# Kernel optimization log

Hardware: AMD Instinct MI355X
Metric: run time of the kernel (lower is better)

## Reference

```python
import jax, jax.numpy as jnp
import numpy as np
from jax import lax

B, T, IN, H, NC = 512, 512, 128, 256, 10
GRID_SIZE, SPLINE_ORDER = 5, 3


def _grid(in_f):
    h = 2.0 / GRID_SIZE
    pts = jnp.arange(-SPLINE_ORDER, GRID_SIZE + SPLINE_ORDER + 1, dtype=jnp.float32) * h - 1.0
    return jnp.broadcast_to(pts, (in_f, pts.shape[0]))


def _b_splines(x, grid):
    # x: (B, in); grid: (in, GRID_SIZE + 2*SPLINE_ORDER + 1)
    xg = x[..., None]
    b = ((xg >= grid[:, :-1]) & (xg < grid[:, 1:])).astype(x.dtype)
    for k in range(1, SPLINE_ORDER + 1):
        b = ((xg - grid[:, :-(k + 1)]) / (grid[:, k:-1] - grid[:, :-(k + 1)]) * b[..., :-1]
             + (grid[:, k + 1:] - xg) / (grid[:, k + 1:] - grid[:, 1:-k]) * b[..., 1:])
    return b  # (B, in, GRID_SIZE + SPLINE_ORDER)


def _kan_linear(x, base_w, spline_w, scaler):
    g = _grid(x.shape[-1])
    base = jax.nn.silu(x) @ base_w.T
    spline = jnp.einsum('bik,oik->bo', _b_splines(x, g), spline_w * scaler[..., None])
    return base + spline


def _gru_cell(x, h, wih, whh, bih, bhh):
    gi = x @ wih.T + bih
    gh = h @ whh.T + bhh
    ir, iz, inn = jnp.split(gi, 3, axis=-1)
    hr, hz, hn = jnp.split(gh, 3, axis=-1)
    r = jax.nn.sigmoid(ir + hr)
    z = jax.nn.sigmoid(iz + hz)
    n = jnp.tanh(inn + r * hn)
    return (1.0 - z) * n + z * h


def _lstm_single(x, wih, whh, bih, bhh):
    # single-timestep LSTM with zero initial (h, c); gate order i,f,g,o
    h0 = jnp.zeros((x.shape[0], whh.shape[1]), x.dtype)
    g = x @ wih.T + h0 @ whh.T + bih + bhh
    i, f, gg, o = jnp.split(g, 4, axis=-1)
    c = jax.nn.sigmoid(i) * jnp.tanh(gg)
    return jax.nn.sigmoid(o) * jnp.tanh(c)


def setup_inputs() -> dict:
    keys = iter(jax.random.split(jax.random.key(0), 64))
    def w(*shape):
        return jax.random.normal(next(keys), shape, jnp.float32) * 0.1
    d = {}
    d['x'] = jax.random.normal(next(keys), (B, T, IN), jnp.float32)
    d['gru0_wih'] = w(3 * H, IN); d['gru0_whh'] = w(3 * H, H)
    d['gru0_bih'] = w(3 * H); d['gru0_bhh'] = w(3 * H)
    d['gru1_wih'] = w(3 * H, H); d['gru1_whh'] = w(3 * H, H)
    d['gru1_bih'] = w(3 * H); d['gru1_bhh'] = w(3 * H)
    for suf in ['0', '0r', '1', '1r']:
        d['lw_ih' + suf] = w(512, 256); d['lw_hh' + suf] = w(512, 128)
        d['lb_ih' + suf] = w(512); d['lb_hh' + suf] = w(512)
    d['kan1_base'] = w(64, 256); d['kan1_spline'] = w(64, 256, GRID_SIZE + SPLINE_ORDER); d['kan1_scaler'] = w(64, 256)
    d['kan2_base'] = w(NC, 64); d['kan2_spline'] = w(NC, 64, GRID_SIZE + SPLINE_ORDER); d['kan2_scaler'] = w(NC, 64)
    return d


def reference(x, gru0_wih, gru0_whh, gru0_bih, gru0_bhh, gru1_wih, gru1_whh, gru1_bih, gru1_bhh,
              lw_ih0, lw_hh0, lb_ih0, lb_hh0, lw_ih0r, lw_hh0r, lb_ih0r, lb_hh0r,
              lw_ih1, lw_hh1, lb_ih1, lb_hh1, lw_ih1r, lw_hh1r, lb_ih1r, lb_hh1r,
              kan1_base, kan1_spline, kan1_scaler, kan2_base, kan2_spline, kan2_scaler):
    bsz = x.shape[0]
    h_init = (jnp.zeros((bsz, H), x.dtype), jnp.zeros((bsz, H), x.dtype))

    def step(carry, xt):
        h0, h1 = carry
        h0 = _gru_cell(xt, h0, gru0_wih, gru0_whh, gru0_bih, gru0_bhh)
        h1 = _gru_cell(h0, h1, gru1_wih, gru1_whh, gru1_bih, gru1_bhh)
        return (h0, h1), None

    (h0, h1), _ = lax.scan(step, h_init, jnp.swapaxes(x, 0, 1))  # time-major scan
    s = h1  # last layer final hidden, seq_len-1 single step for LSTM
    o0 = jnp.concatenate([_lstm_single(s, lw_ih0, lw_hh0, lb_ih0, lb_hh0),
                          _lstm_single(s, lw_ih0r, lw_hh0r, lb_ih0r, lb_hh0r)], axis=-1)
    o1 = jnp.concatenate([_lstm_single(o0, lw_ih1, lw_hh1, lb_ih1, lb_hh1),
                          _lstm_single(o0, lw_ih1r, lw_hh1r, lb_ih1r, lb_hh1r)], axis=-1)
    z = _kan_linear(o1, kan1_base, kan1_spline, kan1_scaler)
    return _kan_linear(z, kan2_base, kan2_spline, kan2_scaler)
```

## Files before the change

kernel.cpp:

```cpp
#include <hip/hip_runtime.h>
#include <stdint.h>


constexpr int B_  = 512;
constexpr int T_  = 512;
constexpr int IN_ = 128;
constexpr int H_  = 256;
constexpr int GR_ = 32;
constexpr int PL_ = GR_ * 2 * 4096;
constexpr int TCp = 64;
constexpr int NCp = 8;

typedef __attribute__((ext_vector_type(8))) short bf16x8;
typedef __attribute__((ext_vector_type(4))) float f32x4;

#define MFMA16(a, b, c) __builtin_amdgcn_mfma_f32_16x16x32_bf16((a), (b), (c), 0, 0, 0)

__device__ __forceinline__ float bf2f(unsigned short u){
    union { unsigned int i; float f; } v; v.i = ((unsigned int)u) << 16; return v.f;
}
__device__ __forceinline__ unsigned short f2bf(float f){
    union { float f; unsigned int i; } v; v.f = f;
    return (unsigned short)((v.i + 0x7FFFu + ((v.i >> 16) & 1u)) >> 16);
}
__device__ __forceinline__ unsigned int cvtpk(float a, float b){
    unsigned int r;
    asm("v_cvt_pk_bf16_f32 %0, %1, %2" : "=v"(r) : "v"(a), "v"(b));
    return r;
}
__device__ __forceinline__ unsigned long long pk4(float a, float b, float c, float d){
    const unsigned int lo = cvtpk(a, b), hi = cvtpk(c, d);
    return (unsigned long long)lo | ((unsigned long long)hi << 32);
}
__device__ __forceinline__ float sig_(float x){
    return __builtin_amdgcn_rcpf(1.0f + __expf(-x));
}
__device__ __forceinline__ float tanh_(float x){
    return 1.0f - 2.0f * __builtin_amdgcn_rcpf(1.0f + __expf(2.0f * x));
}
__device__ __forceinline__ bf16x8 ldb8g(const unsigned short* p){ return *(const bf16x8*)p; }

union U64x2 { unsigned long long q[2]; bf16x8 v; };

__device__ __forceinline__ void gl2lds16(const void* g, void* l){
    __builtin_amdgcn_global_load_lds(
        (const __attribute__((address_space(1))) unsigned int*)g,
        (__attribute__((address_space(3))) unsigned int*)l, 16, 0, 0);
}

__global__ void srt_detect(const unsigned int* __restrict__ xw, unsigned int* __restrict__ flag){
    int cnt = 0;
    for (int i = threadIdx.x; i < 1024; i += 64){
        const unsigned int lo = xw[i] & 0xFFFFu;
        const int e = (int)((lo >> 7) & 0xFFu);
        if (e >= 100 && e <= 140) cnt++;
    }
    #pragma unroll
    for (int o = 32; o > 0; o >>= 1) cnt += __shfl_down(cnt, o);
    if (threadIdx.x == 0) *flag = (cnt > 614) ? 1u : 0u;
}

struct ConvTab { const void* src[26]; int n[26]; int off[26]; };

__global__ __launch_bounds__(256) void srt_conv(ConvTab ct, unsigned short* __restrict__ wb,
                                                const unsigned int* __restrict__ flag){
    const bool isb = (*flag != 0);
    const int gsz = gridDim.x * blockDim.x;
    const int gid = blockIdx.x * blockDim.x + threadIdx.x;
    for (int j = 0; j < 26; ++j){
        const int n = ct.n[j];
        unsigned short* o = wb + ct.off[j];
        if (isb){
            const unsigned short* s = (const unsigned short*)ct.src[j];
            for (int i = gid; i < n; i += gsz) o[i] = s[i];
        } else {
            const float* s = (const float*)ct.src[j];
            for (int i = gid; i < n; i += gsz) o[i] = f2bf(s[i]);
        }
    }
}

__global__ __launch_bounds__(256) void srt_prep(
    float* __restrict__ h0s, float* __restrict__ h1s,
    float* __restrict__ bias0, float* __restrict__ bias1,
    const unsigned short* __restrict__ b0ih, const unsigned short* __restrict__ b0hh,
    const unsigned short* __restrict__ b1ih, const unsigned short* __restrict__ b1hh,
    unsigned int* __restrict__ seq)
{
    const int gid = blockIdx.x * blockDim.x + threadIdx.x;
    h0s[gid] = 0.f;
    h1s[gid] = 0.f;
    if (gid < 768){
        bias0[gid] = bf2f(b0ih[gid]) + (gid < 512 ? bf2f(b0hh[gid]) : 0.f);
        bias1[gid] = bf2f(b1ih[gid]) + (gid < 512 ? bf2f(b1hh[gid]) : 0.f);
    }
    if (gid < 1024) seq[gid] = 0u;
}

__device__ void seq_dev(unsigned short* shm,
    const unsigned short* __restrict__ gi,
    const unsigned short* __restrict__ whh,
    const unsigned short* __restrict__ bhh,
    float* __restrict__ hstate,
    unsigned short* __restrict__ h_all,
    const int TC, const int bg)
{
    unsigned short* wnL   = shm;
    unsigned short* hbufB = shm + 32768;
    unsigned short* gibB  = shm + 32768 + 8192;

    const int tid  = threadIdx.x;
    const int lane = tid & 63;
    const int wv   = tid >> 6;
    const int l15  = lane & 15;
    const int quad = lane >> 4;
    const int m0   = bg * 16;
    const int swz  = (l15 & 7) << 4;

    bf16x8 wr[5][8];
    #pragma unroll
    for (int fi = 0; fi < 6; ++fi){
        const int u = fi >> 1, ii = fi & 1;
        const unsigned short* wp =
            whh + (size_t)(u * 256 + wv * 32 + ii * 16 + l15) * 256 + quad * 8;
        if (fi < 5){
            #pragma unroll
            for (int kc = 0; kc < 8; ++kc) wr[fi][kc] = ldb8g(wp + kc * 32);
        } else {
            #pragma unroll
            for (int kc = 0; kc < 8; ++kc)
                *(bf16x8*)&wnL[((wv * 8 + kc) << 9) + lane * 8] = ldb8g(wp + kc * 32);
        }
    }

    f32x4 bn0[2];
    #pragma unroll
    for (int ii = 0; ii < 2; ++ii)
        #pragma unroll
        for (int j = 0; j < 4; ++j)
            bn0[ii][j] = bf2f(bhh[512 + wv * 32 + ii * 16 + quad * 4 + j]);

    f32x4 hr[2];
    #pragma unroll
    for (int ii = 0; ii < 2; ++ii)
        hr[ii] = *(const f32x4*)&hstate[(size_t)(m0 + l15) * 256 + wv * 32 + ii * 16 + quad * 4];

    const unsigned short* gpp[3]; int gdl[3];
    #pragma unroll
    for (int i = 0; i < 3; ++i){
        const int g_  = i * 512 + tid;
        const int row = g_ / 96;
        const int cg  = g_ - row * 96;
        gpp[i] = gi + ((size_t)m0 + row) * 768 + ((cg ^ (row & 7)) << 3);
        gdl[i] = g_ * 8;
    }

    #pragma unroll
    for (int ii = 0; ii < 2; ++ii){
        const unsigned long long pk = pk4(hr[ii][0], hr[ii][1], hr[ii][2], hr[ii][3]);
        *(unsigned long long*)((char*)hbufB + l15 * 512 +
            ((wv * 64 + ii * 32 + quad * 8) ^ swz)) = pk;
    }
    #pragma unroll
    for (int i = 0; i < 3; ++i) gl2lds16(gpp[i], &gibB[gdl[i]]);
    __syncthreads();

    #pragma unroll 1
    for (int t = 0; t < TC; ++t){
        const int par = t & 1;
        unsigned short* hb_cur = hbufB + par * 4096;
        unsigned short* hb_nxt = hbufB + (par ^ 1) * 4096;
        unsigned short* gb_cur = gibB + par * 12288;
        unsigned short* gb_nxt = gibB + (par ^ 1) * 12288;

        if (t + 1 < TC){
            const size_t toff = (size_t)(t + 1) * (512 * 768);
            #pragma unroll
            for (int i = 0; i < 3; ++i) gl2lds16(gpp[i] + toff, &gb_nxt[gdl[i]]);
        }

        f32x4 aR0 = {0,0,0,0}, aR1 = {0,0,0,0}, aZ0 = {0,0,0,0}, aZ1 = {0,0,0,0};
        f32x4 aN0 = bn0[0], aN1 = bn0[1];
        __builtin_amdgcn_s_setprio(1);
        #pragma unroll
        for (int kc = 0; kc < 8; ++kc){
            const bf16x8 hb = *(const bf16x8*)((const char*)hb_cur +
                l15 * 512 + ((kc * 64 + quad * 16) ^ swz));
            const bf16x8 w5 = *(const bf16x8*)&wnL[((wv * 8 + kc) << 9) + lane * 8];
            aR0 = MFMA16(wr[0][kc], hb, aR0);
            aR1 = MFMA16(wr[1][kc], hb, aR1);
            aZ0 = MFMA16(wr[2][kc], hb, aZ0);
            aZ1 = MFMA16(wr[3][kc], hb, aZ1);
            aN0 = MFMA16(wr[4][kc], hb, aN0);
            aN1 = MFMA16(w5,        hb, aN1);
        }
        __builtin_amdgcn_s_setprio(0);

        const char* gbase = (const char*)gb_cur + l15 * 1536;
        #pragma unroll
        for (int ii = 0; ii < 2; ++ii){
            const int cb = wv * 64 + ii * 32 + quad * 8;
            const unsigned long long qr = *(const unsigned long long*)(gbase + ((       cb) ^ swz));
            const unsigned long long qz = *(const unsigned long long*)(gbase + ((512  + cb) ^ swz));
            const unsigned long long qn = *(const unsigned long long*)(gbase + ((1024 + cb) ^ swz));
            const f32x4 aR = ii ? aR1 : aR0;
            const f32x4 aZ = ii ? aZ1 : aZ0;
            const f32x4 aN = ii ? aN1 : aN0;
            #pragma unroll
            for (int j = 0; j < 4; ++j){
                const float rr = sig_(aR[j] + bf2f((unsigned short)(qr >> (16 * j))));
                const float zz = sig_(aZ[j] + bf2f((unsigned short)(qz >> (16 * j))));
                const float nn = tanh_(bf2f((unsigned short)(qn >> (16 * j))) + rr * aN[j]);
                hr[ii][j] = (1.0f - zz) * nn + zz * hr[ii][j];
            }
        }

        #pragma unroll
        for (int ii = 0; ii < 2; ++ii){
            const unsigned long long pk = pk4(hr[ii][0], hr[ii][1], hr[ii][2], hr[ii][3]);
            *(unsigned long long*)((char*)hb_nxt + l15 * 512 +
                ((wv * 64 + ii * 32 + quad * 8) ^ swz)) = pk;
            if (h_all)
                *(unsigned long long*)(h_all + ((size_t)t * 512 + m0 + l15) * 256 +
                    wv * 32 + ii * 16 + quad * 4) = pk;
        }

        __syncthreads();
    }

    #pragma unroll
    for (int ii = 0; ii < 2; ++ii)
        *(f32x4*)&hstate[(size_t)(m0 + l15) * 256 + wv * 32 + ii * 16 + quad * 4] = hr[ii];
}

template<int K, bool XS>
__device__ void gemm_dev(unsigned short* shm, const void* Asrc, const bool isb,
                         const int t0, const unsigned short* __restrict__ W,
                         const float* __restrict__ bias,
                         unsigned short* __restrict__ C,
                         const int nb, const int mg)
{
    unsigned short* Wt = shm;
    unsigned short* Ab = shm + 64 * K;

    const int tid = threadIdx.x;
    const int lane = tid & 63, wv = tid >> 6;
    const int l15 = lane & 15, quad = lane >> 4;
    const int fh = wv & 1, mq = wv >> 1;
    constexpr int NK  = K / 64;
    constexpr int GW  = K / 8;
    constexpr int WG  = 64 * GW / 512;
    constexpr int NIT = 32 * NK;

    #pragma unroll
    for (int i = 0; i < WG; ++i){
        const int g_ = i * 512 + tid;
        const int row = g_ / GW, cg = g_ % GW;
        gl2lds16(W + (size_t)(nb * 64 + row) * K + ((cg ^ (row & 7)) << 3), &Wt[g_ * 8]);
    }

    float bs[2][4];
    #pragma unroll
    for (int ni = 0; ni < 2; ++ni)
        #pragma unroll
        for (int j = 0; j < 4; ++j)
            bs[ni][j] = bias[nb * 64 + fh * 32 + ni * 16 + quad * 4 + j];

    auto stageA = [&](int it){
        const int mt = it / NK, kk = it % NK;
        unsigned short* dst = Ab + (it & 1) * 8192;
        #pragma unroll
        for (int i = 0; i < 2; ++i){
            const int g_ = i * 512 + tid;
            const int row = g_ >> 3, cg = g_ & 7;
            const int r = mg * 4096 + mt * 128 + row;
            if (XS){
                const int b = r & 511, tt = r >> 9;
                const size_t s0 = ((size_t)b * 512 + (t0 + tt)) * 128 + kk * 64;
                if (isb){
                    gl2lds16((const unsigned short*)Asrc + s0 + ((cg ^ (row & 7)) << 3),
                             &dst[g_ * 8]);
                } else {
                    const float* p = (const float*)Asrc + s0 + cg * 8;
                    const float4 f0 = *(const float4*)p;
                    const float4 f1 = *(const float4*)(p + 4);
                    uint4 u;
                    u.x = cvtpk(f0.x, f0.y); u.y = cvtpk(f0.z, f0.w);
                    u.z = cvtpk(f1.x, f1.y); u.w = cvtpk(f1.z, f1.w);
                    *(uint4*)&dst[(row * 8 + (cg ^ (row & 7))) * 8] = u;
                }
            } else {
                gl2lds16((const unsigned short*)Asrc + (size_t)r * K + kk * 64 +
                         ((cg ^ (row & 7)) << 3), &dst[g_ * 8]);
            }
        }
    };

    stageA(0);
    __syncthreads();

    bf16x8 wf[2][2 * NK];
    #pragma unroll
    for (int ni = 0; ni < 2; ++ni)
        #pragma unroll
        for (int k2 = 0; k2 < 2 * NK; ++k2){
            const int rf = fh * 32 + ni * 16 + l15;
            wf[ni][k2] = *(const bf16x8*)((const char*)Wt +
                rf * (2 * K) + (((k2 * 4 + quad) ^ (rf & 7)) << 4));
        }

    #pragma unroll 1
    for (int mt = 0; mt < 32; ++mt){
        f32x4 acc[2][2];
        #pragma unroll
        for (int ni = 0; ni < 2; ++ni){
            acc[ni][0] = (f32x4){0,0,0,0};
            acc[ni][1] = (f32x4){0,0,0,0};
        }

        #pragma unroll
        for (int kk = 0; kk < NK; ++kk){
            const int it = mt * NK + kk;
            if (it) __syncthreads();
            if (it + 1 < NIT) stageA(it + 1);

            const char* ab = (const char*)(Ab + (it & 1) * 8192);
            #pragma unroll
            for (int kc = 0; kc < 2; ++kc){
                bf16x8 af[2];
                #pragma unroll
                for (int mi = 0; mi < 2; ++mi){
                    const int ra = mq * 32 + mi * 16 + l15;
                    af[mi] = *(const bf16x8*)(ab + ra * 128 +
                              (((kc * 4 + quad) ^ (ra & 7)) << 4));
                }
                #pragma unroll
                for (int ni = 0; ni < 2; ++ni)
                    #pragma unroll
                    for (int mi = 0; mi < 2; ++mi)
                        acc[ni][mi] = MFMA16(wf[ni][kk * 2 + kc], af[mi], acc[ni][mi]);
            }
        }

        #pragma unroll
        for (int ni = 0; ni < 2; ++ni)
            #pragma unroll
            for (int mi = 0; mi < 2; ++mi){
                const unsigned int lo = cvtpk(acc[ni][mi][0] + bs[ni][0],
                                              acc[ni][mi][1] + bs[ni][1]);
                const unsigned int hi = cvtpk(acc[ni][mi][2] + bs[ni][2],
                                              acc[ni][mi][3] + bs[ni][3]);
                const int row = mg * 4096 + mt * 128 + mq * 32 + mi * 16 + l15;
                const int col = nb * 64 + fh * 32 + ni * 16 + quad * 4;
                uint2 st; st.x = lo; st.y = hi;
                *(uint2*)(C + (size_t)row * 768 + col) = st;
            }
    }
}

struct PA {
    const void* xv;
    const unsigned int* flag;
    const unsigned short *w0ih, *w0hh, *b0hh, *w1ih, *w1hh, *b1hh;
    const float *bias0, *bias1;
    float *h0s, *h1s;
    unsigned short *gi0a, *gi0b, *haa, *hab, *gi1a, *gi1b;
    int p;
};

__global__ __launch_bounds__(512, 1) void srt_phase(PA a){
    __shared__ __align__(16) unsigned short shm[65536];
    const int bid = blockIdx.x;
    const int p = a.p;

    if (bid < 32){
        const int c = p - 1; if (c < 0 || c >= NCp) return;
        seq_dev(shm, (c & 1) ? a.gi0b : a.gi0a, a.w0hh, a.b0hh, a.h0s,
                (c & 1) ? a.hab : a.haa, TCp, bid);
    } else if (bid < 64){
        const int c = p - 3; if (c < 0 || c >= NCp) return;
        seq_dev(shm, (c & 1) ? a.gi1b : a.gi1a, a.w1hh, a.b1hh, a.h1s,
                nullptr, TCp, bid - 32);
    } else if (bid < 160){
        const int c = p; if (c >= NCp) return;
        const bool isb = (*a.flag != 0);
        const int idx = bid - 64;
        gemm_dev<128, true>(shm, a.xv, isb, c * TCp, a.w0ih, a.bias0,
                            (c & 1) ? a.gi0b : a.gi0a, idx % 12, idx / 12);
    } else {
        const int c = p - 2; if (c < 0 || c >= NCp) return;
        const int idx = bid - 160;
        gemm_dev<256, false>(shm, (c & 1) ? a.hab : a.haa, true, 0, a.w1ih, a.bias1,
                             (c & 1) ? a.gi1b : a.gi1a, idx % 12, idx / 12);
    }
}

__global__ __launch_bounds__(256, 1) void srt_gru(
    const void* __restrict__ xv,
    const unsigned short* __restrict__ w0ih,
    const unsigned short* __restrict__ w0hh,
    const unsigned short* __restrict__ b0ih,
    const unsigned short* __restrict__ b0hh,
    const unsigned short* __restrict__ w1ih,
    const unsigned short* __restrict__ w1hh,
    const unsigned short* __restrict__ b1ih,
    const unsigned short* __restrict__ b1hh,
    float* __restrict__ s_out,
    const unsigned int* __restrict__ flagp,
    unsigned int* __restrict__ seq,
    unsigned short* __restrict__ hb)
{
    __shared__ __align__(16) unsigned short w0hhL[4 * 24 * 512];

    const bool isb = (*flagp != 0);
    const int tid  = threadIdx.x;
    const int lane = tid & 63;
    const int wv   = tid >> 6;
    const int l15  = lane & 15;
    const int quad = lane >> 4;
    const int q    = blockIdx.x >> 5;
    const int g    = blockIdx.x & 31;
    const int m0   = g * 16;
    const int c    = q * 64 + wv * 16 + l15;

    bf16x8 w0ihr[3][4];
    #pragma unroll
    for (int u = 0; u < 3; ++u)
        #pragma unroll
        for (int kc = 0; kc < 4; ++kc)
            w0ihr[u][kc] = ldb8g(w0ih + (u * 256 + c) * IN_ + kc * 32 + quad * 8);

    bf16x8 w1ihr[3][8], w1hhr[3][8];
    #pragma unroll
    for (int u = 0; u < 3; ++u)
        #pragma unroll
        for (int kc = 0; kc < 8; ++kc){
            w1ihr[u][kc] = ldb8g(w1ih + (u * 256 + c) * H_ + kc * 32 + quad * 8);
            w1hhr[u][kc] = ldb8g(w1hh + (u * 256 + c) * H_ + kc * 32 + quad * 8);
        }

    const int wl = wv * 12288 + lane * 8;
    #pragma unroll
    for (int u = 0; u < 3; ++u)
        #pragma unroll
        for (int kc = 0; kc < 8; ++kc){
            const bf16x8 f = ldb8g(w0hh + (u * 256 + c) * H_ + kc * 32 + quad * 8);
            *(bf16x8*)&w0hhL[wl + (u * 8 + kc) * 512] = f;
        }

    const float brz0a = bf2f(b0ih[c])       + bf2f(b0hh[c]);
    const float brz0b = bf2f(b0ih[256 + c]) + bf2f(b0hh[256 + c]);
    const float bni0v = bf2f(b0ih[512 + c]);
    const float bnh0v = bf2f(b0hh[512 + c]);
    const float brz1a = bf2f(b1ih[c])       + bf2f(b1hh[c]);
    const float brz1b = bf2f(b1ih[256 + c]) + bf2f(b1hh[256 + c]);
    const float bni1v = bf2f(b1ih[512 + c]);
    const float bnh1v = bf2f(b1hh[512 + c]);
    __syncthreads();

    float h0r[4] = {0.f, 0.f, 0.f, 0.f};
    float h1r[4] = {0.f, 0.f, 0.f, 0.f};

    const size_t xrow = (size_t)(m0 + l15) * (T_ * IN_) + quad * 8;
    const unsigned short* pxb = (const unsigned short*)xv + xrow;
    const float*          pxf = (const float*)xv + xrow;

    unsigned int* sq = seq + g * 32;
    const int wr_row[4] = {(quad * 4 + 0) * 256 + c, (quad * 4 + 1) * 256 + c,
                           (quad * 4 + 2) * 256 + c, (quad * 4 + 3) * 256 + c};

    const f32x4 z4 = {0.f, 0.f, 0.f, 0.f};
    bf16x8 h0A[8], h1A[8];
    #pragma unroll
    for (int kc = 0; kc < 8; ++kc){
        h0A[kc] = (bf16x8)(short)0;
        h1A[kc] = (bf16x8)(short)0;
    }

    #pragma unroll 1
    for (int t = 0; t < T_; ++t){
        const int par = t & 1;
        const unsigned int tgt = 4u * (unsigned)(t + 1);
        unsigned short* plane = hb + par * PL_ + g * (2 * 4096);

        #pragma unroll
        for (int j = 0; j < 4; ++j)
            __hip_atomic_store(&plane[4096 + wr_row[j]], f2bf(h1r[j]),
                               __ATOMIC_RELAXED, __HIP_MEMORY_SCOPE_AGENT);

        bf16x8 ax[4];
        if (isb){
            #pragma unroll
            for (int kc = 0; kc < 4; ++kc) ax[kc] = ldb8g(pxb + t * IN_ + kc * 32);
        } else {
            #pragma unroll
            for (int kc = 0; kc < 4; ++kc){
                const float* p = pxf + t * IN_ + kc * 32;
                const float4 f0 = *(const float4*)p;
                const float4 f1 = *(const float4*)(p + 4);
                bf16x8 a;
                a[0] = (short)f2bf(f0.x); a[1] = (short)f2bf(f0.y);
                a[2] = (short)f2bf(f0.z); a[3] = (short)f2bf(f0.w);
                a[4] = (short)f2bf(f1.x); a[5] = (short)f2bf(f1.y);
                a[6] = (short)f2bf(f1.z); a[7] = (short)f2bf(f1.w);
                ax[kc] = a;
            }
        }

        f32x4 Tr = z4, Tz = z4, Tni = z4, Tnh = z4;
        #pragma unroll
        for (int kc = 0; kc < 4; ++kc){
            Tr  = MFMA16(ax[kc], w0ihr[0][kc], Tr);
            Tz  = MFMA16(ax[kc], w0ihr[1][kc], Tz);
            Tni = MFMA16(ax[kc], w0ihr[2][kc], Tni);
        }
        #pragma unroll
        for (int kc = 0; kc < 8; ++kc){
            const bf16x8 a = h0A[kc];
            Tr  = MFMA16(a, *(const bf16x8*)&w0hhL[wl + (0 * 8 + kc) * 512], Tr);
            Tz  = MFMA16(a, *(const bf16x8*)&w0hhL[wl + (1 * 8 + kc) * 512], Tz);
            Tnh = MFMA16(a, *(const bf16x8*)&w0hhL[wl + (2 * 8 + kc) * 512], Tnh);
        }
        #pragma unroll
        for (int j = 0; j < 4; ++j){
            const float rr = sig_(Tr[j] + brz0a);
            const float zz = sig_(Tz[j] + brz0b);
            const float nn = tanh_(Tni[j] + bni0v + rr * (Tnh[j] + bnh0v));
            h0r[j] = (1.0f - zz) * nn + zz * h0r[j];
        }

        #pragma unroll
        for (int j = 0; j < 4; ++j)
            __hip_atomic_store(&plane[wr_row[j]], f2bf(h0r[j]),
                               __ATOMIC_RELAXED, __HIP_MEMORY_SCOPE_AGENT);

        __syncthreads();
        if (tid == 0)
            __hip_atomic_fetch_add(sq, 1u, __ATOMIC_RELAXED, __HIP_MEMORY_SCOPE_AGENT);
        if (lane == 0){
            while (__hip_atomic_load(sq, __ATOMIC_RELAXED, __HIP_MEMORY_SCOPE_AGENT) < tgt)
                __builtin_amdgcn_s_sleep(1);
        }
        __atomic_signal_fence(__ATOMIC_ACQ_REL);

        {
            const unsigned short* r0 = plane + l15 * 256 + quad * 8;
            #pragma unroll
            for (int kc = 0; kc < 8; ++kc){
                U64x2 u0, u1;
                u0.q[0] = __hip_atomic_load((const unsigned long long*)(r0 + kc * 32),
                                            __ATOMIC_RELAXED, __HIP_MEMORY_SCOPE_AGENT);
                u0.q[1] = __hip_atomic_load((const unsigned long long*)(r0 + kc * 32 + 4),
                                            __ATOMIC_RELAXED, __HIP_MEMORY_SCOPE_AGENT);
                u1.q[0] = __hip_atomic_load((const unsigned long long*)(r0 + 4096 + kc * 32),
                                            __ATOMIC_RELAXED, __HIP_MEMORY_SCOPE_AGENT);
                u1.q[1] = __hip_atomic_load((const unsigned long long*)(r0 + 4096 + kc * 32 + 4),
                                            __ATOMIC_RELAXED, __HIP_MEMORY_SCOPE_AGENT);
                h0A[kc] = u0.v;
                h1A[kc] = u1.v;
            }
        }

        Tr = z4; Tz = z4; Tni = z4; Tnh = z4;
        #pragma unroll
        for (int kc = 0; kc < 8; ++kc){
            const bf16x8 a0 = h0A[kc];
            const bf16x8 a1 = h1A[kc];
            Tr  = MFMA16(a0, w1ihr[0][kc], Tr);
            Tr  = MFMA16(a1, w1hhr[0][kc], Tr);
            Tz  = MFMA16(a0, w1ihr[1][kc], Tz);
            Tz  = MFMA16(a1, w1hhr[1][kc], Tz);
            Tni = MFMA16(a0, w1ihr[2][kc], Tni);
            Tnh = MFMA16(a1, w1hhr[2][kc], Tnh);
        }
        #pragma unroll
        for (int j = 0; j < 4; ++j){
            const float rr = sig_(Tr[j] + brz1a);
            const float zz = sig_(Tz[j] + brz1b);
            const float nn = tanh_(Tni[j] + bni1v + rr * (Tnh[j] + bnh1v));
            h1r[j] = (1.0f - zz) * nn + zz * h1r[j];
        }
    }

    #pragma unroll
    for (int j = 0; j < 4; ++j)
        s_out[(size_t)(m0 + quad * 4 + j) * H_ + c] = h1r[j];
}

__device__ __forceinline__ float knot_(int p){ return (float)(p - 3) * 0.4f - 1.0f; }

__device__ __forceinline__ void bspline8(float xv, float* bb8){
    float bb[11];
    #pragma unroll
    for (int p = 0; p < 11; ++p)
        bb[p] = (xv >= knot_(p) && xv < knot_(p + 1)) ? 1.f : 0.f;
    #pragma unroll
    for (int k = 1; k <= 3; ++k){
        #pragma unroll
        for (int p = 0; p <= 10 - k; ++p){
            const float tp = knot_(p), tpk = knot_(p + k);
            const float tp1 = knot_(p + 1), tpk1 = knot_(p + k + 1);
            bb[p] = (xv - tp) / (tpk - tp) * bb[p] + (tpk1 - xv) / (tpk1 - tp1) * bb[p + 1];
        }
    }
    #pragma unroll
    for (int j = 0; j < 8; ++j) bb8[j] = bb[j];
}

__device__ __forceinline__ void lstm_part(const float* sxv, const unsigned short* w,
                                          int uu, int k0, float* out3){
    const unsigned short* wi = w + (size_t)uu * 256 + k0;
    const unsigned short* wg = w + (size_t)(256 + uu) * 256 + k0;
    const unsigned short* wo = w + (size_t)(384 + uu) * 256 + k0;
    float ai = 0.f, ag = 0.f, ao = 0.f;
    for (int k = 0; k < 64; k += 8){
        const bf16x8 vi = ldb8g(wi + k);
        const bf16x8 vg = ldb8g(wg + k);
        const bf16x8 vo = ldb8g(wo + k);
        #pragma unroll
        for (int j = 0; j < 8; ++j){
            const float s = sxv[k0 + k + j];
            ai += bf2f((unsigned short)vi[j]) * s;
            ag += bf2f((unsigned short)vg[j]) * s;
            ao += bf2f((unsigned short)vo[j]) * s;
        }
    }
    out3[0] = ai; out3[1] = ag; out3[2] = ao;
}

__global__ __launch_bounds__(1024) void srt_tail(
    const float* __restrict__ in,
    const unsigned short* __restrict__ w0f, const unsigned short* __restrict__ bi0f,
    const unsigned short* __restrict__ bh0f,
    const unsigned short* __restrict__ w0r, const unsigned short* __restrict__ bi0r,
    const unsigned short* __restrict__ bh0r,
    const unsigned short* __restrict__ w1f, const unsigned short* __restrict__ bi1f,
    const unsigned short* __restrict__ bh1f,
    const unsigned short* __restrict__ w1r, const unsigned short* __restrict__ bi1r,
    const unsigned short* __restrict__ bh1r,
    const unsigned short* __restrict__ k1b, const unsigned short* __restrict__ k1s,
    const unsigned short* __restrict__ k1c,
    const unsigned short* __restrict__ k2b, const unsigned short* __restrict__ k2s,
    const unsigned short* __restrict__ k2c,
    void* __restrict__ outp,
    const unsigned int* __restrict__ flagp)
{
    __shared__ float sx[256];
    __shared__ float sy[256];
    __shared__ float part[4][256][3];
    __shared__ float sil[256];
    __shared__ float spl[256][8];
    __shared__ float red16[64][16];
    __shared__ float sil2[64];
    __shared__ float spl2[64][8];
    __shared__ float red2[10][16];

    const int b = blockIdx.x, tid = threadIdx.x;
    const int qr = tid >> 8, sub = tid & 255;
    const int dir = sub >> 7, uu = sub & 127;

    if (tid < 256) sx[tid] = in[b * 256 + tid];
    __syncthreads();

    float p3[3];
    lstm_part(sx, dir ? w0r : w0f, uu, qr * 64, p3);
    part[qr][sub][0] = p3[0]; part[qr][sub][1] = p3[1]; part[qr][sub][2] = p3[2];
    __syncthreads();
    if (tid < 256){
        const unsigned short* bi = dir ? bi0r : bi0f;
        const unsigned short* bh = dir ? bh0r : bh0f;
        const float ai = part[0][sub][0] + part[1][sub][0] + part[2][sub][0] + part[3][sub][0];
        const float ag = part[0][sub][1] + part[1][sub][1] + part[2][sub][1] + part[3][sub][1];
        const float ao = part[0][sub][2] + part[1][sub][2] + part[2][sub][2] + part[3][sub][2];
        const float gi = ai + bf2f(bi[uu])       + bf2f(bh[uu]);
        const float gg = ag + bf2f(bi[256 + uu]) + bf2f(bh[256 + uu]);
        const float go = ao + bf2f(bi[384 + uu]) + bf2f(bh[384 + uu]);
        sy[sub] = sig_(go) * tanh_(sig_(gi) * tanh_(gg));
    }
    __syncthreads();

    lstm_part(sy, dir ? w1r : w1f, uu, qr * 64, p3);
    part[qr][sub][0] = p3[0]; part[qr][sub][1] = p3[1]; part[qr][sub][2] = p3[2];
    __syncthreads();
    if (tid < 256){
        const unsigned short* bi = dir ? bi1r : bi1f;
        const unsigned short* bh = dir ? bh1r : bh1f;
        const float ai = part[0][sub][0] + part[1][sub][0] + part[2][sub][0] + part[3][sub][0];
        const float ag = part[0][sub][1] + part[1][sub][1] + part[2][sub][1] + part[3][sub][1];
        const float ao = part[0][sub][2] + part[1][sub][2] + part[2][sub][2] + part[3][sub][2];
        const float gi = ai + bf2f(bi[uu])       + bf2f(bh[uu]);
        const float gg = ag + bf2f(bi[256 + uu]) + bf2f(bh[256 + uu]);
        const float go = ao + bf2f(bi[384 + uu]) + bf2f(bh[384 + uu]);
        const float o1v = sig_(go) * tanh_(sig_(gi) * tanh_(gg));
        sil[sub] = o1v * sig_(o1v);
        float bb[8];
        bspline8(o1v, bb);
        #pragma unroll
        for (int j = 0; j < 8; ++j) spl[sub][j] = bb[j];
    }
    __syncthreads();

    {
        const int o = tid >> 4, q16 = tid & 15;
        float acc = 0.f;
        for (int k = q16 * 16; k < q16 * 16 + 16; ++k){
            acc += sil[k] * bf2f(k1b[o * 256 + k]);
            float t = 0.f;
            #pragma unroll
            for (int j = 0; j < 8; ++j) t += spl[k][j] * bf2f(k1s[(o * 256 + k) * 8 + j]);
            acc += t * bf2f(k1c[o * 256 + k]);
        }
        red16[o][q16] = acc;
    }
    __syncthreads();
    if (tid < 64){
        float zv = 0.f;
        #pragma unroll
        for (int i = 0; i < 16; ++i) zv += red16[tid][i];
        sil2[tid] = zv * sig_(zv);
        float b2[8];
        bspline8(zv, b2);
        #pragma unroll
        for (int j = 0; j < 8; ++j) spl2[tid][j] = b2[j];
    }
    __syncthreads();

    if (tid < 160){
        const int o2 = tid >> 4, q = tid & 15;
        float a2 = 0.f;
        for (int k = q * 4; k < q * 4 + 4; ++k){
            a2 += sil2[k] * bf2f(k2b[o2 * 64 + k]);
            float t = 0.f;
            #pragma unroll
            for (int j = 0; j < 8; ++j) t += spl2[k][j] * bf2f(k2s[(o2 * 64 + k) * 8 + j]);
            a2 += t * bf2f(k2c[o2 * 64 + k]);
        }
        red2[o2][q] = a2;
    }
    __syncthreads();
    if (tid < 10){
        float a2 = 0.f;
        #pragma unroll
        for (int i = 0; i < 16; ++i) a2 += red2[tid][i];
        if (*flagp) ((unsigned short*)outp)[b * 10 + tid] = f2bf(a2);
        else        ((float*)outp)[b * 10 + tid] = a2;
    }
}

extern "C" void kernel_launch(void* const* d_in, const int* in_sizes, int n_in,
                              void* d_out, int out_size, void* d_ws, size_t ws_size,
                              hipStream_t stream)
{
    unsigned int* flag = (unsigned int*)d_ws;
    float* s = (float*)((char*)d_ws + 16);
    unsigned short* wb = (unsigned short*)(s + 512 * 256);

    const int idxs[26] = {1,2,3,4,5,6,7,8, 9,11,12, 13,15,16, 17,19,20, 21,23,24,
                          25,26,27, 28,29,30};
    ConvTab ct;
    int off = 0;
    int offs[26];
    for (int j = 0; j < 26; ++j){
        ct.src[j] = d_in[idxs[j]];
        ct.n[j]   = in_sizes[idxs[j]];
        ct.off[j] = off;
        offs[j]   = off;
        off += in_sizes[idxs[j]];
    }
    uintptr_t p = (uintptr_t)(wb + off);
    p = (p + 255) & ~(uintptr_t)255;
    unsigned int* seq = (unsigned int*)p;
    unsigned short* hb = (unsigned short*)(seq + 1024);
    p = (uintptr_t)(hb + 2 * 32 * 2 * 4096);
    p = (p + 255) & ~(uintptr_t)255;
    float* h0s   = (float*)p;
    float* bias0 = h0s + 512 * 256;
    float* bias1 = bias0 + 768;
    p = (uintptr_t)(bias1 + 768);
    p = (p + 255) & ~(uintptr_t)255;
    char* dyn = (char*)p;
    const size_t used = (size_t)(dyn - (char*)d_ws);

    const size_t slab_gi = (size_t)TCp * 512 * 768;
    const size_t slab_ha = (size_t)TCp * 512 * 256;
    const size_t pipe_need = used + (4 * slab_gi + 2 * slab_ha) * sizeof(unsigned short);
    const bool pipe_ok = pipe_need <= ws_size;

    const unsigned short *w0ih = wb + offs[0],  *w0hh = wb + offs[1];
    const unsigned short *b0ih = wb + offs[2],  *b0hh = wb + offs[3];
    const unsigned short *w1ih = wb + offs[4],  *w1hh = wb + offs[5];
    const unsigned short *b1ih = wb + offs[6],  *b1hh = wb + offs[7];
    const unsigned short *lwih0  = wb + offs[8],  *lbih0  = wb + offs[9],  *lbhh0  = wb + offs[10];
    const unsigned short *lwih0r = wb + offs[11], *lbih0r = wb + offs[12], *lbhh0r = wb + offs[13];
    const unsigned short *lwih1  = wb + offs[14], *lbih1  = wb + offs[15], *lbhh1  = wb + offs[16];
    const unsigned short *lwih1r = wb + offs[17], *lbih1r = wb + offs[18], *lbhh1r = wb + offs[19];
    const unsigned short *k1b = wb + offs[20], *k1s = wb + offs[21], *k1c = wb + offs[22];
    const unsigned short *k2b = wb + offs[23], *k2s = wb + offs[24], *k2c = wb + offs[25];

    srt_detect<<<1, 64, 0, stream>>>((const unsigned int*)d_in[0], flag);
    srt_conv<<<1024, 256, 0, stream>>>(ct, wb, flag);
    srt_prep<<<512, 256, 0, stream>>>(h0s, s, bias0, bias1, b0ih, b0hh, b1ih, b1hh, seq);

    if (pipe_ok){
        unsigned short* gi0a = (unsigned short*)dyn;
        unsigned short* gi0b = gi0a + slab_gi;
        unsigned short* haa  = gi0b + slab_gi;
        unsigned short* hab  = haa + slab_ha;
        unsigned short* gi1a = hab + slab_ha;
        unsigned short* gi1b = gi1a + slab_gi;

        PA a;
        a.xv = d_in[0]; a.flag = flag;
        a.w0ih = w0ih; a.w0hh = w0hh; a.b0hh = b0hh;
        a.w1ih = w1ih; a.w1hh = w1hh; a.b1hh = b1hh;
        a.bias0 = bias0; a.bias1 = bias1;
        a.h0s = h0s; a.h1s = s;
        a.gi0a = gi0a; a.gi0b = gi0b; a.haa = haa; a.hab = hab;
        a.gi1a = gi1a; a.gi1b = gi1b;
        for (int ph = 0; ph <= NCp + 2; ++ph){
            a.p = ph;
            srt_phase<<<256, 512, 0, stream>>>(a);
        }
    } else {
        srt_gru<<<128, 256, 0, stream>>>(d_in[0], w0ih, w0hh, b0ih, b0hh,
                                         w1ih, w1hh, b1ih, b1hh, s, flag, seq, hb);
    }

    srt_tail<<<512, 1024, 0, stream>>>(s,
        lwih0, lbih0, lbhh0, lwih0r, lbih0r, lbhh0r,
        lwih1, lbih1, lbhh1, lwih1r, lbih1r, lbhh1r,
        k1b, k1s, k1c, k2b, k2s, k2c, d_out, flag);
}
```

Measured before the change: 1.851 ms.

## Pre-convert input to time-major bf16 and triple-buffer async LDS loads

Adds a kernel that converts x to bf16 in time-major layout once, so the layer-0 input GEMM can use direct global-to-LDS async loads instead of per-element fp32 conversion through registers. Both the recurrent sequence loop and the GEMM A-tile staging move from double to triple buffering with a prefetch distance of two. They replace __syncthreads with explicit vmcnt waits plus s_barrier so loads stay in flight across iterations. This costs an extra pass over x, more workspace and more LDS, and relies on hand-counted vmcnt values being correct.

```diff
diff --git a/kernel.cpp b/kernel.cpp
--- a/kernel.cpp
+++ b/kernel.cpp
@@ -97,6 +97,36 @@
     if (gid < 1024) seq[gid] = 0u;
 }
 
+__global__ __launch_bounds__(256) void srt_xconv(
+    const void* __restrict__ xv, unsigned short* __restrict__ xb,
+    const unsigned int* __restrict__ flagp)
+{
+    const bool isb = (*flagp != 0);
+    const int total = 512 * 512 * 16;
+    const int gsz = gridDim.x * blockDim.x;
+    for (int g_ = blockIdx.x * blockDim.x + threadIdx.x; g_ < total; g_ += gsz){
+        const int tt  = g_ >> 13;
+        const int rem = g_ & 8191;
+        const int b = rem >> 4, cg = rem & 15;
+        const long long s8 = ((long long)b * 512 + tt) * 16 + cg;
+        bf16x8 v;
+        if (isb){
+            v = ((const bf16x8*)xv)[s8];
+        } else {
+            const float* p = (const float*)xv + s8 * 8;
+            const float4 f0 = *(const float4*)p;
+            const float4 f1 = *(const float4*)(p + 4);
+            unsigned int u0 = cvtpk(f0.x, f0.y), u1 = cvtpk(f0.z, f0.w);
+            unsigned int u2 = cvtpk(f1.x, f1.y), u3 = cvtpk(f1.z, f1.w);
+            U64x2 w;
+            w.q[0] = (unsigned long long)u0 | ((unsigned long long)u1 << 32);
+            w.q[1] = (unsigned long long)u2 | ((unsigned long long)u3 << 32);
+            v = w.v;
+        }
+        ((bf16x8*)xb)[g_] = v;
+    }
+}
+
 __device__ void seq_dev(unsigned short* shm,
     const unsigned short* __restrict__ gi,
     const unsigned short* __restrict__ whh,
@@ -107,7 +137,7 @@
 {
     unsigned short* wnL   = shm;
     unsigned short* hbufB = shm + 32768;
-    unsigned short* gibB  = shm + 32768 + 8192;
+    unsigned short* gibB  = shm + 40960;
 
     const int tid  = threadIdx.x;
     const int lane = tid & 63;
@@ -163,20 +193,32 @@
     }
     #pragma unroll
     for (int i = 0; i < 3; ++i) gl2lds16(gpp[i], &gibB[gdl[i]]);
-    __syncthreads();
+    #pragma unroll
+    for (int i = 0; i < 3; ++i) gl2lds16(gpp[i] + (size_t)(512 * 768), &gibB[12288 + gdl[i]]);
 
     #pragma unroll 1
     for (int t = 0; t < TC; ++t){
         const int par = t & 1;
         unsigned short* hb_cur = hbufB + par * 4096;
         unsigned short* hb_nxt = hbufB + (par ^ 1) * 4096;
-        unsigned short* gb_cur = gibB + par * 12288;
-        unsigned short* gb_nxt = gibB + (par ^ 1) * 12288;
-
-        if (t + 1 < TC){
-            const size_t toff = (size_t)(t + 1) * (512 * 768);
-            #pragma unroll
-            for (int i = 0; i < 3; ++i) gl2lds16(gpp[i] + toff, &gb_nxt[gdl[i]]);
+        unsigned short* gb_cur = gibB + (t % 3) * 12288;
+
+        if (h_all){
+            if (t >= 2)      asm volatile("s_waitcnt vmcnt(10) lgkmcnt(0)" ::: "memory");
+            else if (t == 1) asm volatile("s_waitcnt vmcnt(8) lgkmcnt(0)" ::: "memory");
+            else             asm volatile("s_waitcnt vmcnt(6) lgkmcnt(0)" ::: "memory");
+        } else {
+            asm volatile("s_waitcnt vmcnt(6) lgkmcnt(0)" ::: "memory");
+        }
+        __builtin_amdgcn_s_barrier();
+        __builtin_amdgcn_sched_barrier(0);
+
+        {
+            const int ts = (t + 2 < TC) ? (t + 2) : (TC - 1);
+            unsigned short* gb_pre = gibB + ((t + 2) % 3) * 12288;
+            const size_t toff = (size_t)ts * (512 * 768);
+            #pragma unroll
+            for (int i = 0; i < 3; ++i) gl2lds16(gpp[i] + toff, &gb_pre[gdl[i]]);
         }
 
         f32x4 aR0 = {0,0,0,0}, aR1 = {0,0,0,0}, aZ0 = {0,0,0,0}, aZ1 = {0,0,0,0};
@@ -224,24 +266,23 @@
                 *(unsigned long long*)(h_all + ((size_t)t * 512 + m0 + l15) * 256 +
                     wv * 32 + ii * 16 + quad * 4) = pk;
         }
-
-        __syncthreads();
-    }
+    }
+    asm volatile("s_waitcnt vmcnt(0)" ::: "memory");
 
     #pragma unroll
     for (int ii = 0; ii < 2; ++ii)
         *(f32x4*)&hstate[(size_t)(m0 + l15) * 256 + wv * 32 + ii * 16 + quad * 4] = hr[ii];
 }
 
-template<int K, bool XS>
-__device__ void gemm_dev(unsigned short* shm, const void* Asrc, const bool isb,
-                         const int t0, const unsigned short* __restrict__ W,
+template<int K>
+__device__ void gemm_dev(unsigned short* shm, const unsigned short* __restrict__ A,
+                         const unsigned short* __restrict__ W,
                          const float* __restrict__ bias,
                          unsigned short* __restrict__ C,
                          const int nb, const int mg)
 {
     unsigned short* Wt = shm;
-    unsigned short* Ab = shm + 64 * K;
+    unsigned short* Ab = shm + 16384;
 
     const int tid = threadIdx.x;
     const int lane = tid & 63, wv = tid >> 6;
@@ -266,38 +307,23 @@
         for (int j = 0; j < 4; ++j)
             bs[ni][j] = bias[nb * 64 + fh * 32 + ni * 16 + quad * 4 + j];
 
-    auto stageA = [&](int it){
-        const int mt = it / NK, kk = it % NK;
-        unsigned short* dst = Ab + (it & 1) * 8192;
+    auto stageA = [&](int ic, int slot){
+        const int mt = ic / NK, kk = ic % NK;
+        unsigned short* dst = Ab + slot * 8192;
         #pragma unroll
         for (int i = 0; i < 2; ++i){
             const int g_ = i * 512 + tid;
             const int row = g_ >> 3, cg = g_ & 7;
-            const int r = mg * 4096 + mt * 128 + row;
-            if (XS){
-                const int b = r & 511, tt = r >> 9;
-                const size_t s0 = ((size_t)b * 512 + (t0 + tt)) * 128 + kk * 64;
-                if (isb){
-                    gl2lds16((const unsigned short*)Asrc + s0 + ((cg ^ (row & 7)) << 3),
-                             &dst[g_ * 8]);
-                } else {
-                    const float* p = (const float*)Asrc + s0 + cg * 8;
-                    const float4 f0 = *(const float4*)p;
-                    const float4 f1 = *(const float4*)(p + 4);
-                    uint4 u;
-                    u.x = cvtpk(f0.x, f0.y); u.y = cvtpk(f0.z, f0.w);
-                    u.z = cvtpk(f1.x, f1.y); u.w = cvtpk(f1.z, f1.w);
-                    *(uint4*)&dst[(row * 8 + (cg ^ (row & 7))) * 8] = u;
-                }
-            } else {
-                gl2lds16((const unsigned short*)Asrc + (size_t)r * K + kk * 64 +
-                         ((cg ^ (row & 7)) << 3), &dst[g_ * 8]);
-            }
+            gl2lds16(A + (size_t)(mg * 4096 + mt * 128 + row) * K + kk * 64 +
+                     ((cg ^ (row & 7)) << 3), &dst[g_ * 8]);
         }
     };
 
-    stageA(0);
-    __syncthreads();
+    stageA(0, 0);
+    stageA(1, 1);
+    asm volatile("s_waitcnt vmcnt(4)" ::: "memory");
+    __builtin_amdgcn_s_barrier();
+    __builtin_amdgcn_sched_barrier(0);
 
     bf16x8 wf[2][2 * NK];
     #pragma unroll
@@ -321,10 +347,13 @@
         #pragma unroll
         for (int kk = 0; kk < NK; ++kk){
             const int it = mt * NK + kk;
-            if (it) __syncthreads();
-            if (it + 1 < NIT) stageA(it + 1);
-
-            const char* ab = (const char*)(Ab + (it & 1) * 8192);
+            if (it >= 2 && kk < 2) asm volatile("s_waitcnt vmcnt(10)" ::: "memory");
+            else                   asm volatile("s_waitcnt vmcnt(2)"  ::: "memory");
+            __builtin_amdgcn_s_barrier();
+            __builtin_amdgcn_sched_barrier(0);
+            stageA((it + 2 < NIT) ? (it + 2) : (NIT - 1), (it + 2) % 3);
+
+            const char* ab = (const char*)(Ab + (it % 3) * 8192);
             #pragma unroll
             for (int kc = 0; kc < 2; ++kc){
                 bf16x8 af[2];
@@ -356,11 +385,11 @@
                 *(uint2*)(C + (size_t)row * 768 + col) = st;
             }
     }
+    asm volatile("s_waitcnt vmcnt(0)" ::: "memory");
 }
 
 struct PA {
-    const void* xv;
-    const unsigned int* flag;
+    const unsigned short* xb;
     const unsigned short *w0ih, *w0hh, *b0hh, *w1ih, *w1hh, *b1hh;
     const float *bias0, *bias1;
     float *h0s, *h1s;
@@ -369,7 +398,7 @@
 };
 
 __global__ __launch_bounds__(512, 1) void srt_phase(PA a){
-    __shared__ __align__(16) unsigned short shm[65536];
+    __shared__ __align__(16) unsigned short shm[77824];
     const int bid = blockIdx.x;
     const int p = a.p;
 
@@ -383,15 +412,14 @@
                 nullptr, TCp, bid - 32);
     } else if (bid < 160){
         const int c = p; if (c >= NCp) return;
-        const bool isb = (*a.flag != 0);
         const int idx = bid - 64;
-        gemm_dev<128, true>(shm, a.xv, isb, c * TCp, a.w0ih, a.bias0,
-                            (c & 1) ? a.gi0b : a.gi0a, idx % 12, idx / 12);
+        gemm_dev<128>(shm, a.xb + (size_t)c * (TCp * 512 * 128), a.w0ih, a.bias0,
+                      (c & 1) ? a.gi0b : a.gi0a, idx % 12, idx / 12);
     } else {
         const int c = p - 2; if (c < 0 || c >= NCp) return;
         const int idx = bid - 160;
-        gemm_dev<256, false>(shm, (c & 1) ? a.hab : a.haa, true, 0, a.w1ih, a.bias1,
-                             (c & 1) ? a.gi1b : a.gi1a, idx % 12, idx / 12);
+        gemm_dev<256>(shm, (c & 1) ? a.hab : a.haa, a.w1ih, a.bias1,
+                      (c & 1) ? a.gi1b : a.gi1a, idx % 12, idx / 12);
     }
 }
 
@@ -781,9 +809,10 @@
     char* dyn = (char*)p;
     const size_t used = (size_t)(dyn - (char*)d_ws);
 
-    const size_t slab_gi = (size_t)TCp * 512 * 768;
-    const size_t slab_ha = (size_t)TCp * 512 * 256;
-    const size_t pipe_need = used + (4 * slab_gi + 2 * slab_ha) * sizeof(unsigned short);
+    const size_t xb_sz    = (size_t)512 * 512 * 128;
+    const size_t slab_gi  = (size_t)TCp * 512 * 768;
+    const size_t slab_ha  = (size_t)TCp * 512 * 256;
+    const size_t pipe_need = used + (xb_sz + 4 * slab_gi + 2 * slab_ha) * sizeof(unsigned short);
     const bool pipe_ok = pipe_need <= ws_size;
 
     const unsigned short *w0ih = wb + offs[0],  *w0hh = wb + offs[1];
@@ -802,15 +831,18 @@
     srt_prep<<<512, 256, 0, stream>>>(h0s, s, bias0, bias1, b0ih, b0hh, b1ih, b1hh, seq);
 
     if (pipe_ok){
-        unsigned short* gi0a = (unsigned short*)dyn;
+        unsigned short* xb   = (unsigned short*)dyn;
+        unsigned short* gi0a = xb + xb_sz;
         unsigned short* gi0b = gi0a + slab_gi;
         unsigned short* haa  = gi0b + slab_gi;
         unsigned short* hab  = haa + slab_ha;
         unsigned short* gi1a = hab + slab_ha;
         unsigned short* gi1b = gi1a + slab_gi;
 
+        srt_xconv<<<2048, 256, 0, stream>>>(d_in[0], xb, flag);
+
         PA a;
-        a.xv = d_in[0]; a.flag = flag;
+        a.xb = xb;
         a.w0ih = w0ih; a.w0hh = w0hh; a.b0hh = b0hh;
         a.w1ih = w1ih; a.w1hh = w1hh; a.b1hh = b1hh;
         a.bias0 = bias0; a.bias1 = bias1;
```

Measured after the change: 1.777 ms. 1.04x faster.
